# Kernel tuning notes

Hardware: AMD Instinct MI355X
Metric: run time of the kernel (lower is better)

The kernel has to match this reference:

```python
import jax, jax.numpy as jnp
import numpy as np

N = 50000      # nodes
E = 800000     # edges (avg degree 16)
VOCAB = 300    # in_dim = config['vocab_size']
EMBED = 256    # embed_dim
FC = 128       # fc_dim
NCLS = 4       # n_classes_stance
EPS = 1e-12    # F.normalize eps


def setup_inputs() -> dict:
    key = jax.random.key(0)
    ks = jax.random.split(key, 13)
    s_in = 1.0 / np.sqrt(VOCAB)
    s_h = 1.0 / np.sqrt(EMBED)
    s_fc = 1.0 / np.sqrt(FC)
    return {
        "x": jax.random.normal(ks[0], (N, VOCAB), jnp.float32),
        "edge_index": jax.random.randint(ks[1], (2, E), 0, N, dtype=jnp.int32),
        "node_mask": jnp.ones((N, 1), dtype=bool),
        # SAGEConv 1: lin_l (neighbor, with bias) and lin_r (root, no bias)
        "w1_l": jax.random.normal(ks[2], (EMBED, VOCAB), jnp.float32) * s_in,
        "b1_l": jnp.zeros((EMBED,), jnp.float32),
        "w1_r": jax.random.normal(ks[3], (EMBED, VOCAB), jnp.float32) * s_in,
        # SAGEConv 2
        "w2_l": jax.random.normal(ks[4], (EMBED, EMBED), jnp.float32) * s_h,
        "b2_l": jnp.zeros((EMBED,), jnp.float32),
        "w2_r": jax.random.normal(ks[5], (EMBED, EMBED), jnp.float32) * s_h,
        # classifier_stance MLP
        "cw1": jax.random.normal(ks[6], (FC, EMBED), jnp.float32) * s_h,
        "cb1": jnp.zeros((FC,), jnp.float32),
        "cw2": jax.random.normal(ks[7], (NCLS, FC), jnp.float32) * s_fc,
        "cb2": jnp.zeros((NCLS,), jnp.float32),
    }


def _sage_conv(x, src, dst, w_l, b_l, w_r):
    # mean aggregation of source-node features onto destinations
    msg = x[src]                                              # [E, d] gather
    s = jax.ops.segment_sum(msg, dst, num_segments=N)         # [N, d] scatter-add
    cnt = jax.ops.segment_sum(jnp.ones((src.shape[0], 1), x.dtype), dst,
                              num_segments=N)                 # [N, 1]
    agg = s / jnp.maximum(cnt, 1.0)
    h = agg @ w_l.T + b_l + x @ w_r.T                         # lin_l(agg)+lin_r(x)
    # normalize=True -> L2 normalize rows (F.normalize semantics)
    n = jnp.linalg.norm(h, axis=-1, keepdims=True)
    return h / jnp.maximum(n, EPS)


def reference(x, edge_index, node_mask, w1_l, b1_l, w1_r, w2_l, b2_l, w2_r,
              cw1, cb1, cw2, cb2):
    # eval mode: node_drop mask not applied, dropout is identity
    src, dst = edge_index[0], edge_index[1]
    h = jax.nn.relu(_sage_conv(x, src, dst, w1_l, b1_l, w1_r))
    h2 = _sage_conv(h, src, dst, w2_l, b2_l, w2_r)
    out = jax.nn.relu(h2 @ cw1.T + cb1) @ cw2.T + cb2         # classifier_stance
    return (out, node_mask, h2)
```

## Files before the change

kernel.cpp:

```cpp
#include <hip/hip_runtime.h>

constexpr int NN = 50000;
constexpr int MP = 50048;
constexpr int NE = 800000;
constexpr int KV = 300;
constexpr int KP1 = 320;
constexpr int DE = 256;
constexpr int DF = 128;
constexpr int NC = 4;

typedef __attribute__((ext_vector_type(8))) short bf16x8;
typedef __attribute__((ext_vector_type(4))) float f32x4;

__device__ inline float b2f(ushort u) { return __uint_as_float((uint)u << 16); }
__device__ inline ushort f2b(float f) {
    uint u = __float_as_uint(f);
    u += 0x7fffu + ((u >> 16) & 1u);
    return (ushort)(u >> 16);
}
__device__ inline void gload_lds16(const void* g, void* l) {
    __builtin_amdgcn_global_load_lds(
        (const __attribute__((address_space(1))) void*)g,
        (__attribute__((address_space(3))) void*)l, 16, 0, 0);
}

__global__ __launch_bounds__(256) void k_degree(const int* __restrict__ dst,
                                                int* __restrict__ deg) {
    int e = blockIdx.x * 256 + threadIdx.x;
    if (e < NE) atomicAdd(&deg[dst[e]], 1);
}

__global__ __launch_bounds__(256) void k_scan1(const int* __restrict__ deg,
                                               int* __restrict__ partial) {
    __shared__ int sd[256];
    int t = threadIdx.x;
    int n = blockIdx.x * 256 + t;
    sd[t] = (n < NN) ? deg[n] : 0;
    __syncthreads();
    for (int off = 128; off > 0; off >>= 1) {
        if (t < off) sd[t] += sd[t + off];
        __syncthreads();
    }
    if (t == 0) partial[blockIdx.x] = sd[0];
}

__global__ __launch_bounds__(256) void k_scan2(const int* __restrict__ partial,
                                               int* __restrict__ poff, int nb) {
    __shared__ int sd[256];
    int t = threadIdx.x;
    int v = (t < nb) ? partial[t] : 0;
    sd[t] = v;
    __syncthreads();
    for (int off = 1; off < 256; off <<= 1) {
        int x = (t >= off) ? sd[t - off] : 0;
        __syncthreads();
        sd[t] += x;
        __syncthreads();
    }
    poff[t] = sd[t] - v;
}

__global__ __launch_bounds__(256) void k_scan3(const int* __restrict__ deg,
                                               const int* __restrict__ poff,
                                               int* __restrict__ rowptr) {
    __shared__ int sd[256];
    int t = threadIdx.x;
    int n = blockIdx.x * 256 + t;
    int v = (n < NN) ? deg[n] : 0;
    sd[t] = v;
    __syncthreads();
    for (int off = 1; off < 256; off <<= 1) {
        int x = (t >= off) ? sd[t - off] : 0;
        __syncthreads();
        sd[t] += x;
        __syncthreads();
    }
    if (n < NN) rowptr[n] = poff[blockIdx.x] + sd[t] - v;
    if (blockIdx.x == 0 && t == 0) rowptr[NN] = NE;
}

__global__ __launch_bounds__(256) void k_scatter(const int* __restrict__ src,
                                                 const int* __restrict__ dst,
                                                 const int* __restrict__ rowptr,
                                                 int* __restrict__ cnt2,
                                                 int* __restrict__ col) {
    int e = blockIdx.x * 256 + threadIdx.x;
    if (e < NE) {
        int d = dst[e];
        int p = rowptr[d] + atomicAdd(&cnt2[d], 1);
        col[p] = src[e];
    }
}

__global__ __launch_bounds__(256) void k_cvt_x(const float* __restrict__ x,
                                               ushort* __restrict__ xb) {
    int i = blockIdx.x * 256 + threadIdx.x;
    if (i >= MP * (KP1 / 8)) return;
    int row = i / (KP1 / 8);
    int kb = (i % (KP1 / 8)) * 8;
    float f[8] = {0.f, 0.f, 0.f, 0.f, 0.f, 0.f, 0.f, 0.f};
    if (row < NN) {
        const float* s = x + (size_t)row * KV + kb;
        if (kb + 8 <= KV) {
            float4 v0 = *(const float4*)s;
            float4 v1 = *(const float4*)(s + 4);
            f[0] = v0.x; f[1] = v0.y; f[2] = v0.z; f[3] = v0.w;
            f[4] = v1.x; f[5] = v1.y; f[6] = v1.z; f[7] = v1.w;
        } else {
#pragma unroll
            for (int j = 0; j < 8; ++j)
                if (kb + j < KV) f[j] = s[j];
        }
    }
    ushort v[8];
#pragma unroll
    for (int j = 0; j < 8; ++j) v[j] = f2b(f[j]);
    uint4 pk;
    pk.x = (uint)v[0] | ((uint)v[1] << 16);
    pk.y = (uint)v[2] | ((uint)v[3] << 16);
    pk.z = (uint)v[4] | ((uint)v[5] << 16);
    pk.w = (uint)v[6] | ((uint)v[7] << 16);
    *(uint4*)(xb + (size_t)row * KP1 + kb) = pk;
}

__global__ __launch_bounds__(256) void k_cvt_wall(const float* __restrict__ w1l,
                                                  const float* __restrict__ w1r,
                                                  const float* __restrict__ w2l,
                                                  const float* __restrict__ w2r,
                                                  const float* __restrict__ cw1,
                                                  ushort* __restrict__ wcat1,
                                                  ushort* __restrict__ wcat2,
                                                  ushort* __restrict__ cw1b) {
    int i = blockIdx.x * 256 + threadIdx.x;
    const float* src; ushort* dst; int row, kb, Kin;
    if (i < 10240)            { int g = i;          row = g / 40; kb = (g % 40) * 8; src = w1l; dst = wcat1;                       Kin = KV; }
    else if (i < 20480)       { int g = i - 10240;  row = g / 40; kb = (g % 40) * 8; src = w1r; dst = wcat1 + (size_t)256 * KP1;   Kin = KV; }
    else if (i < 28672)       { int g = i - 20480;  row = g / 32; kb = (g % 32) * 8; src = w2l; dst = wcat2;                       Kin = DE; }
    else if (i < 36864)       { int g = i - 28672;  row = g / 32; kb = (g % 32) * 8; src = w2r; dst = wcat2 + (size_t)256 * DE;    Kin = DE; }
    else if (i < 40960)       { int g = i - 36864;  row = g / 32; kb = (g % 32) * 8; src = cw1; dst = cw1b;                        Kin = DE; }
    else return;
    int KPr = (Kin == KV) ? KP1 : DE;
    const float* s = src + (size_t)row * Kin + kb;
    float f[8] = {0.f, 0.f, 0.f, 0.f, 0.f, 0.f, 0.f, 0.f};
    if (kb + 8 <= Kin) {
        float4 v0 = *(const float4*)s;
        float4 v1 = *(const float4*)(s + 4);
        f[0] = v0.x; f[1] = v0.y; f[2] = v0.z; f[3] = v0.w;
        f[4] = v1.x; f[5] = v1.y; f[6] = v1.z; f[7] = v1.w;
    } else {
#pragma unroll
        for (int j = 0; j < 8; ++j)
            if (kb + j < Kin) f[j] = s[j];
    }
    ushort v[8];
#pragma unroll
    for (int j = 0; j < 8; ++j) v[j] = f2b(f[j]);
    uint4 pk;
    pk.x = (uint)v[0] | ((uint)v[1] << 16);
    pk.y = (uint)v[2] | ((uint)v[3] << 16);
    pk.z = (uint)v[4] | ((uint)v[5] << 16);
    pk.w = (uint)v[6] | ((uint)v[7] << 16);
    *(uint4*)(dst + (size_t)row * KPr + kb) = pk;
}

__global__ __launch_bounds__(256) void k_mgemm_layer(const ushort* __restrict__ A,
                                                     const ushort* __restrict__ B,
                                                     unsigned char* __restrict__ ybuf,
                                                     ushort* __restrict__ yrb,
                                                     int KPr) {
    __shared__ __align__(16) ushort As[128 * 64];
    __shared__ __align__(16) ushort Bs[128 * 64];
    const int t = threadIdx.x;
    const int bn = blockIdx.x * 128;
    const int bm = blockIdx.y * 128;
    const int w = t >> 6;
    const int lane = t & 63;
    const int wr = (w >> 1) * 64, wc = (w & 1) * 64;
    const int fr = lane & 15;
    const int fg = lane >> 4;
    const int drow = (lane >> 4) * 4;
    const int dcol = lane & 15;

    f32x4 acc[4][4];
#pragma unroll
    for (int m = 0; m < 4; ++m)
#pragma unroll
        for (int n = 0; n < 4; ++n) acc[m][n] = (f32x4){0.f, 0.f, 0.f, 0.f};

    const int srow = lane >> 3;
    const int sblk = (lane & 7) ^ srow;
    const ushort* Ab = A + (size_t)(bm + w * 32 + srow) * KPr + sblk * 8;
    const ushort* Bb = B + (size_t)(bn + w * 32 + srow) * KPr + sblk * 8;
    ushort* Al = As + w * 2048 + lane * 8;
    ushort* Bl = Bs + w * 2048 + lane * 8;

    for (int k0 = 0; k0 < KPr; k0 += 64) {
#pragma unroll
        for (int j = 0; j < 4; ++j) {
            gload_lds16(Ab + k0 + (size_t)j * 8 * KPr, Al + j * 512);
            gload_lds16(Bb + k0 + (size_t)j * 8 * KPr, Bl + j * 512);
        }
        __syncthreads();
#pragma unroll
        for (int ks = 0; ks < 2; ++ks) {
            bf16x8 af[4], bfr[4];
#pragma unroll
            for (int m = 0; m < 4; ++m) {
                int row = wr + 16 * m + fr;
                int blk = (fg + 4 * ks) ^ (row & 7);
                af[m] = *(const bf16x8*)(As + row * 64 + blk * 8);
            }
#pragma unroll
            for (int n = 0; n < 4; ++n) {
                int row = wc + 16 * n + fr;
                int blk = (fg + 4 * ks) ^ (row & 7);
                bfr[n] = *(const bf16x8*)(Bs + row * 64 + blk * 8);
            }
#pragma unroll
            for (int m = 0; m < 4; ++m)
#pragma unroll
                for (int n = 0; n < 4; ++n)
                    acc[m][n] = __builtin_amdgcn_mfma_f32_16x16x32_bf16(
                        af[m], bfr[n], acc[m][n], 0, 0, 0);
        }
        __syncthreads();
    }
#pragma unroll
    for (int m = 0; m < 4; ++m) {
        int gr0 = bm + wr + 16 * m + drow;
#pragma unroll
        for (int n = 0; n < 4; ++n) {
            int gc = bn + wc + 16 * n + dcol;
#pragma unroll
            for (int r = 0; r < 4; ++r) {
                float v = acc[m][n][r];
                if (gc < 256) {
                    uint p = __builtin_amdgcn_cvt_pk_fp8_f32(v, v, 0, false);
                    ybuf[(size_t)(gr0 + r) * 256 + gc] = (unsigned char)(p & 0xff);
                } else {
                    yrb[(size_t)(gr0 + r) * 256 + (gc - 256)] = f2b(v);
                }
            }
        }
    }
}

__global__ __launch_bounds__(256) void k_mcls(const ushort* __restrict__ A,
                                              const ushort* __restrict__ B,
                                              const float* __restrict__ cb1,
                                              const float* __restrict__ cw2,
                                              const float* __restrict__ cb2,
                                              float* __restrict__ outp) {
    __shared__ __align__(16) ushort smem[128 * 130];
    __shared__ float cw2s[NC * DF];
    ushort* As = smem;
    ushort* Bs = smem + 8192;
    const int t = threadIdx.x;
    const int bm = blockIdx.y * 128;
    const int w = t >> 6;
    const int lane = t & 63;
    const int wr = (w >> 1) * 64, wc = (w & 1) * 64;
    const int fr = lane & 15;
    const int fg = lane >> 4;
    const int drow = (lane >> 4) * 4;
    const int dcol = lane & 15;

    for (int i = t; i < NC * DF; i += 256) cw2s[i] = cw2[i];

    f32x4 acc[4][4];
#pragma unroll
    for (int m = 0; m < 4; ++m)
#pragma unroll
        for (int n = 0; n < 4; ++n) acc[m][n] = (f32x4){0.f, 0.f, 0.f, 0.f};

    const int srow = lane >> 3;
    const int sblk = (lane & 7) ^ srow;
    const ushort* Ab = A + (size_t)(bm + w * 32 + srow) * DE + sblk * 8;
    const ushort* Bb = B + (size_t)(w * 32 + srow) * DE + sblk * 8;
    ushort* Al = As + w * 2048 + lane * 8;
    ushort* Bl = Bs + w * 2048 + lane * 8;

    for (int k0 = 0; k0 < DE; k0 += 64) {
#pragma unroll
        for (int j = 0; j < 4; ++j) {
            gload_lds16(Ab + k0 + (size_t)j * 8 * DE, Al + j * 512);
            gload_lds16(Bb + k0 + (size_t)j * 8 * DE, Bl + j * 512);
        }
        __syncthreads();
#pragma unroll
        for (int ks = 0; ks < 2; ++ks) {
            bf16x8 af[4], bfr[4];
#pragma unroll
            for (int m = 0; m < 4; ++m) {
                int row = wr + 16 * m + fr;
                int blk = (fg + 4 * ks) ^ (row & 7);
                af[m] = *(const bf16x8*)(As + row * 64 + blk * 8);
            }
#pragma unroll
            for (int n = 0; n < 4; ++n) {
                int row = wc + 16 * n + fr;
                int blk = (fg + 4 * ks) ^ (row & 7);
                bfr[n] = *(const bf16x8*)(Bs + row * 64 + blk * 8);
            }
#pragma unroll
            for (int m = 0; m < 4; ++m)
#pragma unroll
                for (int n = 0; n < 4; ++n)
                    acc[m][n] = __builtin_amdgcn_mfma_f32_16x16x32_bf16(
                        af[m], bfr[n], acc[m][n], 0, 0, 0);
        }
        __syncthreads();
    }
#pragma unroll
    for (int m = 0; m < 4; ++m) {
        int lr0 = wr + 16 * m + drow;
#pragma unroll
        for (int n = 0; n < 4; ++n) {
            int f = wc + 16 * n + dcol;
            float bv = cb1[f];
#pragma unroll
            for (int r = 0; r < 4; ++r) {
                float v = fmaxf(acc[m][n][r] + bv, 0.f);
                smem[(lr0 + r) * 130 + f] = f2b(v);
            }
        }
    }
    __syncthreads();
    int node = t >> 1;
    int half = t & 1;
    float p0 = 0.f, p1 = 0.f, p2 = 0.f, p3 = 0.f;
#pragma unroll
    for (int i = 0; i < 32; ++i) {
        uint hv = *(const uint*)&smem[node * 130 + half * 64 + 2 * i];
        float h0 = b2f((ushort)(hv & 0xffff));
        float h1 = b2f((ushort)(hv >> 16));
        int f = half * 64 + 2 * i;
        p0 += h0 * cw2s[0 * DF + f] + h1 * cw2s[0 * DF + f + 1];
        p1 += h0 * cw2s[1 * DF + f] + h1 * cw2s[1 * DF + f + 1];
        p2 += h0 * cw2s[2 * DF + f] + h1 * cw2s[2 * DF + f + 1];
        p3 += h0 * cw2s[3 * DF + f] + h1 * cw2s[3 * DF + f + 1];
    }
    p0 += __shfl_xor(p0, 1, 64);
    p1 += __shfl_xor(p1, 1, 64);
    p2 += __shfl_xor(p2, 1, 64);
    p3 += __shfl_xor(p3, 1, 64);
    int ng = bm + node;
    if (half == 0 && ng < NN) {
        float4 o = make_float4(p0 + cb2[0], p1 + cb2[1], p2 + cb2[2], p3 + cb2[3]);
        *(float4*)(outp + (size_t)ng * NC) = o;
    }
}

__global__ __launch_bounds__(256) void k_aggnorm(const uint* __restrict__ yl,
                                                 const ushort* __restrict__ yrb,
                                                 const float* __restrict__ bias,
                                                 const int* __restrict__ rowptr,
                                                 const int* __restrict__ col,
                                                 float* __restrict__ outf,
                                                 ushort* __restrict__ outb,
                                                 int relu) {
    int wave = threadIdx.x >> 6;
    int lane = threadIdx.x & 63;
    int n = blockIdx.x * 4 + wave;
    if (n >= NN) return;
    int beg = rowptr[n], end = rowptr[n + 1];
    const uint* base = yl + lane;
    float a0 = 0.f, a1 = 0.f, a2 = 0.f, a3 = 0.f;
    float c0 = 0.f, c1 = 0.f, c2 = 0.f, c3 = 0.f;
    int e = beg;
    for (; e + 8 <= end; e += 8) {
        uint v[8];
#pragma unroll
        for (int j = 0; j < 8; ++j) v[j] = base[(size_t)col[e + j] * 64];
#pragma unroll
        for (int j = 0; j < 8; j += 2) {
            a0 += __builtin_amdgcn_cvt_f32_fp8(v[j], 0);
            a1 += __builtin_amdgcn_cvt_f32_fp8(v[j], 1);
            a2 += __builtin_amdgcn_cvt_f32_fp8(v[j], 2);
            a3 += __builtin_amdgcn_cvt_f32_fp8(v[j], 3);
            c0 += __builtin_amdgcn_cvt_f32_fp8(v[j + 1], 0);
            c1 += __builtin_amdgcn_cvt_f32_fp8(v[j + 1], 1);
            c2 += __builtin_amdgcn_cvt_f32_fp8(v[j + 1], 2);
            c3 += __builtin_amdgcn_cvt_f32_fp8(v[j + 1], 3);
        }
    }
    for (; e < end; ++e) {
        uint v = base[(size_t)col[e] * 64];
        a0 += __builtin_amdgcn_cvt_f32_fp8(v, 0);
        a1 += __builtin_amdgcn_cvt_f32_fp8(v, 1);
        a2 += __builtin_amdgcn_cvt_f32_fp8(v, 2);
        a3 += __builtin_amdgcn_cvt_f32_fp8(v, 3);
    }
    a0 += c0; a1 += c1; a2 += c2; a3 += c3;
    int d = end - beg;
    float inv = 1.0f / (float)(d > 1 ? d : 1);
    ushort4 rv = *(const ushort4*)(yrb + (size_t)n * 256 + lane * 4);
    float4 b = *(const float4*)(bias + lane * 4);
    float hx = a0 * inv + b.x + b2f(rv.x);
    float hy = a1 * inv + b.y + b2f(rv.y);
    float hz = a2 * inv + b.z + b2f(rv.z);
    float hw = a3 * inv + b.w + b2f(rv.w);
    float ss = hx * hx + hy * hy + hz * hz + hw * hw;
#pragma unroll
    for (int off = 32; off > 0; off >>= 1) ss += __shfl_xor(ss, off, 64);
    float scale = 1.0f / fmaxf(sqrtf(ss), 1e-12f);
    hx *= scale; hy *= scale; hz *= scale; hw *= scale;
    if (relu) {
        hx = fmaxf(hx, 0.f); hy = fmaxf(hy, 0.f);
        hz = fmaxf(hz, 0.f); hw = fmaxf(hw, 0.f);
    }
    if (outf) {
        float4 o = make_float4(hx, hy, hz, hw);
        *(float4*)(outf + (size_t)n * DE + lane * 4) = o;
    }
    ushort4 ob;
    ob.x = f2b(hx); ob.y = f2b(hy); ob.z = f2b(hz); ob.w = f2b(hw);
    *(ushort4*)(outb + (size_t)n * DE + lane * 4) = ob;
}

__global__ __launch_bounds__(256) void k_mask(const unsigned char* __restrict__ m8,
                                              float* __restrict__ o) {
    int i = blockIdx.x * 256 + threadIdx.x;
    if (i >= NN) return;
    bool bytes = (m8[1] != 0);
    float v;
    if (bytes) v = (m8[i] != 0) ? 1.0f : 0.0f;
    else       v = (((const int*)m8)[i] != 0) ? 1.0f : 0.0f;
    o[i] = v;
}

extern "C" void kernel_launch(void* const* d_in, const int* in_sizes, int n_in,
                              void* d_out, int out_size, void* d_ws, size_t ws_size,
                              hipStream_t stream) {
    const float* x   = (const float*)d_in[0];
    const int*   ei  = (const int*)d_in[1];
    const void*  msk = d_in[2];
    const float* w1l = (const float*)d_in[3];
    const float* b1l = (const float*)d_in[4];
    const float* w1r = (const float*)d_in[5];
    const float* w2l = (const float*)d_in[6];
    const float* b2l = (const float*)d_in[7];
    const float* w2r = (const float*)d_in[8];
    const float* cw1 = (const float*)d_in[9];
    const float* cb1 = (const float*)d_in[10];
    const float* cw2 = (const float*)d_in[11];
    const float* cb2 = (const float*)d_in[12];

    float* out        = (float*)d_out;
    float* out_logits = out;
    float* out_mask   = out + (size_t)NN * NC;
    float* h2f        = out + (size_t)NN * NC + NN;

    char* wp = (char*)d_ws;
    auto alloc = [&](size_t bytes) -> void* {
        void* p = (void*)wp;
        wp += (bytes + 255) & ~(size_t)255;
        return p;
    };
    int* counters = (int*)alloc((size_t)2 * NN * 4);
    int* deg  = counters;
    int* cnt2 = counters + NN;
    int* rowptr  = (int*)alloc((size_t)(NN + 1) * 4);
    int* partial = (int*)alloc(256 * 4);
    int* poff    = (int*)alloc(256 * 4);
    int* col     = (int*)alloc((size_t)NE * 4);
    ushort* xb    = (ushort*)alloc((size_t)MP * KP1 * 2);
    ushort* wcat1 = (ushort*)alloc((size_t)512 * KP1 * 2);
    ushort* wcat2 = (ushort*)alloc((size_t)512 * DE * 2);
    ushort* cw1b  = (ushort*)alloc((size_t)DF * DE * 2);
    unsigned char* ybuf = (unsigned char*)alloc((size_t)MP * 256);
    ushort* yrb   = (ushort*)alloc((size_t)MP * 256 * 2);
    ushort* h1b   = (ushort*)alloc((size_t)MP * DE * 2);
    ushort* h2b   = (ushort*)alloc((size_t)MP * DE * 2);

    const int* srcp = ei;
    const int* dstp = ei + NE;

    hipMemsetAsync(counters, 0, (size_t)2 * NN * 4, stream);
    k_degree<<<(NE + 255) / 256, 256, 0, stream>>>(dstp, deg);
    int nb = (NN + 255) / 256;
    k_scan1<<<nb, 256, 0, stream>>>(deg, partial);
    k_scan2<<<1, 256, 0, stream>>>(partial, poff, nb);
    k_scan3<<<nb, 256, 0, stream>>>(deg, poff, rowptr);
    k_scatter<<<(NE + 255) / 256, 256, 0, stream>>>(srcp, dstp, rowptr, cnt2, col);

    k_cvt_x<<<(MP * (KP1 / 8) + 255) / 256, 256, 0, stream>>>(x, xb);
    k_cvt_wall<<<(40960 + 255) / 256, 256, 0, stream>>>(w1l, w1r, w2l, w2r, cw1,
                                                        wcat1, wcat2, cw1b);

    dim3 g1(512 / 128, MP / 128);
    k_mgemm_layer<<<g1, 256, 0, stream>>>(xb, wcat1, ybuf, yrb, KP1);
    k_aggnorm<<<NN / 4, 256, 0, stream>>>((const uint*)ybuf, yrb, b1l, rowptr, col,
                                          nullptr, h1b, 1);
    k_mgemm_layer<<<g1, 256, 0, stream>>>(h1b, wcat2, ybuf, yrb, DE);
    k_aggnorm<<<NN / 4, 256, 0, stream>>>((const uint*)ybuf, yrb, b2l, rowptr, col,
                                          h2f, h2b, 0);

    dim3 g2(1, MP / 128);
    k_mcls<<<g2, 256, 0, stream>>>(h2b, cw1b, cb1, cw2, cb2, out_logits);
    k_mask<<<(NN + 255) / 256, 256, 0, stream>>>((const unsigned char*)msk, out_mask);
}
```

Before: 401.5 us.

## Fuse independent prep kernels and overlap edge scatter with first GEMM

Merges degree counting with x/weight bf16 conversion into one interleaved launch, and merges the CSR edge scatter, the first-layer GEMM and the mask output into a single kernel whose blocks are interleaved by index. The aim is to cut launch count and let the atomic-bound scatter overlap with compute-bound GEMM tiles instead of running serially. The combined GEMM kernel now reserves shared memory for every block, including the scatter and mask blocks, which may lower occupancy for those blocks.

```diff
diff --git a/kernel.cpp b/kernel.cpp
--- a/kernel.cpp
+++ b/kernel.cpp
@@ -22,12 +22,6 @@
     __builtin_amdgcn_global_load_lds(
         (const __attribute__((address_space(1))) void*)g,
         (__attribute__((address_space(3))) void*)l, 16, 0, 0);
-}
-
-__global__ __launch_bounds__(256) void k_degree(const int* __restrict__ dst,
-                                                int* __restrict__ deg) {
-    int e = blockIdx.x * 256 + threadIdx.x;
-    if (e < NE) atomicAdd(&deg[dst[e]], 1);
 }
 
 __global__ __launch_bounds__(256) void k_scan1(const int* __restrict__ deg,
@@ -79,38 +73,17 @@
     if (blockIdx.x == 0 && t == 0) rowptr[NN] = NE;
 }
 
-__global__ __launch_bounds__(256) void k_scatter(const int* __restrict__ src,
-                                                 const int* __restrict__ dst,
-                                                 const int* __restrict__ rowptr,
-                                                 int* __restrict__ cnt2,
-                                                 int* __restrict__ col) {
-    int e = blockIdx.x * 256 + threadIdx.x;
-    if (e < NE) {
-        int d = dst[e];
-        int p = rowptr[d] + atomicAdd(&cnt2[d], 1);
-        col[p] = src[e];
-    }
-}
-
-__global__ __launch_bounds__(256) void k_cvt_x(const float* __restrict__ x,
-                                               ushort* __restrict__ xb) {
-    int i = blockIdx.x * 256 + threadIdx.x;
-    if (i >= MP * (KP1 / 8)) return;
-    int row = i / (KP1 / 8);
-    int kb = (i % (KP1 / 8)) * 8;
+__device__ inline void cvt8_store(const float* s, int valid, ushort* dptr) {
     float f[8] = {0.f, 0.f, 0.f, 0.f, 0.f, 0.f, 0.f, 0.f};
-    if (row < NN) {
-        const float* s = x + (size_t)row * KV + kb;
-        if (kb + 8 <= KV) {
-            float4 v0 = *(const float4*)s;
-            float4 v1 = *(const float4*)(s + 4);
-            f[0] = v0.x; f[1] = v0.y; f[2] = v0.z; f[3] = v0.w;
-            f[4] = v1.x; f[5] = v1.y; f[6] = v1.z; f[7] = v1.w;
-        } else {
-#pragma unroll
-            for (int j = 0; j < 8; ++j)
-                if (kb + j < KV) f[j] = s[j];
-        }
+    if (valid >= 8) {
+        float4 v0 = *(const float4*)s;
+        float4 v1 = *(const float4*)(s + 4);
+        f[0] = v0.x; f[1] = v0.y; f[2] = v0.z; f[3] = v0.w;
+        f[4] = v1.x; f[5] = v1.y; f[6] = v1.z; f[7] = v1.w;
+    } else {
+#pragma unroll
+        for (int j = 0; j < 8; ++j)
+            if (j < valid) f[j] = s[j];
     }
     ushort v[8];
 #pragma unroll
@@ -120,59 +93,79 @@
     pk.y = (uint)v[2] | ((uint)v[3] << 16);
     pk.z = (uint)v[4] | ((uint)v[5] << 16);
     pk.w = (uint)v[6] | ((uint)v[7] << 16);
-    *(uint4*)(xb + (size_t)row * KP1 + kb) = pk;
-}
-
-__global__ __launch_bounds__(256) void k_cvt_wall(const float* __restrict__ w1l,
-                                                  const float* __restrict__ w1r,
-                                                  const float* __restrict__ w2l,
-                                                  const float* __restrict__ w2r,
-                                                  const float* __restrict__ cw1,
-                                                  ushort* __restrict__ wcat1,
-                                                  ushort* __restrict__ wcat2,
-                                                  ushort* __restrict__ cw1b) {
-    int i = blockIdx.x * 256 + threadIdx.x;
+    *(uint4*)dptr = pk;
+}
+
+__device__ inline void cvt_x_body(int blk, const float* __restrict__ x,
+                                  ushort* __restrict__ xb) {
+    int i = blk * 256 + threadIdx.x;
+    if (i >= MP * (KP1 / 8)) return;
+    int row = i / (KP1 / 8);
+    int kb = (i % (KP1 / 8)) * 8;
+    if (row < NN) {
+        cvt8_store(x + (size_t)row * KV + kb, KV - kb, xb + (size_t)row * KP1 + kb);
+    } else {
+        uint4 z = {0u, 0u, 0u, 0u};
+        *(uint4*)(xb + (size_t)row * KP1 + kb) = z;
+    }
+}
+
+__device__ inline void cvt_wall_body(int blk,
+                                     const float* __restrict__ w1l,
+                                     const float* __restrict__ w1r,
+                                     const float* __restrict__ w2l,
+                                     const float* __restrict__ w2r,
+                                     const float* __restrict__ cw1,
+                                     ushort* __restrict__ wcat1,
+                                     ushort* __restrict__ wcat2,
+                                     ushort* __restrict__ cw1b) {
+    int i = blk * 256 + threadIdx.x;
     const float* src; ushort* dst; int row, kb, Kin;
-    if (i < 10240)            { int g = i;          row = g / 40; kb = (g % 40) * 8; src = w1l; dst = wcat1;                       Kin = KV; }
-    else if (i < 20480)       { int g = i - 10240;  row = g / 40; kb = (g % 40) * 8; src = w1r; dst = wcat1 + (size_t)256 * KP1;   Kin = KV; }
-    else if (i < 28672)       { int g = i - 20480;  row = g / 32; kb = (g % 32) * 8; src = w2l; dst = wcat2;                       Kin = DE; }
-    else if (i < 36864)       { int g = i - 28672;  row = g / 32; kb = (g % 32) * 8; src = w2r; dst = wcat2 + (size_t)256 * DE;    Kin = DE; }
-    else if (i < 40960)       { int g = i - 36864;  row = g / 32; kb = (g % 32) * 8; src = cw1; dst = cw1b;                        Kin = DE; }
+    if (i < 10240)      { int g = i;         row = g / 40; kb = (g % 40) * 8; src = w1l; dst = wcat1;                     Kin = KV; }
+    else if (i < 20480) { int g = i - 10240; row = g / 40; kb = (g % 40) * 8; src = w1r; dst = wcat1 + (size_t)256 * KP1; Kin = KV; }
+    else if (i < 28672) { int g = i - 20480; row = g / 32; kb = (g % 32) * 8; src = w2l; dst = wcat2;                     Kin = DE; }
+    else if (i < 36864) { int g = i - 28672; row = g / 32; kb = (g % 32) * 8; src = w2r; dst = wcat2 + (size_t)256 * DE;  Kin = DE; }
+    else if (i < 40960) { int g = i - 36864; row = g / 32; kb = (g % 32) * 8; src = cw1; dst = cw1b;                      Kin = DE; }
     else return;
     int KPr = (Kin == KV) ? KP1 : DE;
-    const float* s = src + (size_t)row * Kin + kb;
-    float f[8] = {0.f, 0.f, 0.f, 0.f, 0.f, 0.f, 0.f, 0.f};
-    if (kb + 8 <= Kin) {
-        float4 v0 = *(const float4*)s;
-        float4 v1 = *(const float4*)(s + 4);
-        f[0] = v0.x; f[1] = v0.y; f[2] = v0.z; f[3] = v0.w;
-        f[4] = v1.x; f[5] = v1.y; f[6] = v1.z; f[7] = v1.w;
+    cvt8_store(src + (size_t)row * Kin + kb, Kin - kb, dst + (size_t)row * KPr + kb);
+}
+
+__global__ __launch_bounds__(256) void k_prep(const float* __restrict__ x,
+                                              const int* __restrict__ dst,
+                                              const float* __restrict__ w1l,
+                                              const float* __restrict__ w1r,
+                                              const float* __restrict__ w2l,
+                                              const float* __restrict__ w2r,
+                                              const float* __restrict__ cw1,
+                                              ushort* __restrict__ xb,
+                                              ushort* __restrict__ wcat1,
+                                              ushort* __restrict__ wcat2,
+                                              ushort* __restrict__ cw1b,
+                                              int* __restrict__ deg) {
+    int bid = blockIdx.x;
+    int q = bid / 7, r = bid % 7;
+    if (r < 2) {
+        int s = 2 * q + r;
+        if (s < 3125) {
+            int e = s * 256 + threadIdx.x;
+            if (e < NE) atomicAdd(&deg[dst[e]], 1);
+        }
     } else {
-#pragma unroll
-        for (int j = 0; j < 8; ++j)
-            if (kb + j < Kin) f[j] = s[j];
-    }
-    ushort v[8];
-#pragma unroll
-    for (int j = 0; j < 8; ++j) v[j] = f2b(f[j]);
-    uint4 pk;
-    pk.x = (uint)v[0] | ((uint)v[1] << 16);
-    pk.y = (uint)v[2] | ((uint)v[3] << 16);
-    pk.z = (uint)v[4] | ((uint)v[5] << 16);
-    pk.w = (uint)v[6] | ((uint)v[7] << 16);
-    *(uint4*)(dst + (size_t)row * KPr + kb) = pk;
-}
-
-__global__ __launch_bounds__(256) void k_mgemm_layer(const ushort* __restrict__ A,
-                                                     const ushort* __restrict__ B,
-                                                     unsigned char* __restrict__ ybuf,
-                                                     ushort* __restrict__ yrb,
-                                                     int KPr) {
-    __shared__ __align__(16) ushort As[128 * 64];
-    __shared__ __align__(16) ushort Bs[128 * 64];
+        int w = 5 * q + (r - 2);
+        if (w < 7820) cvt_x_body(w, x, xb);
+        else if (w < 7980)
+            cvt_wall_body(w - 7820, w1l, w1r, w2l, w2r, cw1, wcat1, wcat2, cw1b);
+    }
+}
+
+__device__ inline void gemm_layer_body(const ushort* __restrict__ A,
+                                       const ushort* __restrict__ B,
+                                       unsigned char* __restrict__ ybuf,
+                                       ushort* __restrict__ yrb,
+                                       int KPr, int bn, int bm,
+                                       ushort* As, ushort* Bs) {
     const int t = threadIdx.x;
-    const int bn = blockIdx.x * 128;
-    const int bm = blockIdx.y * 128;
     const int w = t >> 6;
     const int lane = t & 63;
     const int wr = (w >> 1) * 64, wc = (w & 1) * 64;
@@ -243,6 +236,125 @@
             }
         }
     }
+}
+
+__global__ __launch_bounds__(256) void k_mgemm_layer(const ushort* __restrict__ A,
+                                                     const ushort* __restrict__ B,
+                                                     unsigned char* __restrict__ ybuf,
+                                                     ushort* __restrict__ yrb,
+                                                     int KPr) {
+    __shared__ __align__(16) ushort As[128 * 64];
+    __shared__ __align__(16) ushort Bs[128 * 64];
+    gemm_layer_body(A, B, ybuf, yrb, KPr, blockIdx.x * 128, blockIdx.y * 128, As, Bs);
+}
+
+__global__ __launch_bounds__(256) void k_g1s(const ushort* __restrict__ A,
+                                             const ushort* __restrict__ B,
+                                             unsigned char* __restrict__ ybuf,
+                                             ushort* __restrict__ yrb,
+                                             const int* __restrict__ src,
+                                             const int* __restrict__ dst,
+                                             const int* __restrict__ rowptr,
+                                             int* __restrict__ cnt2,
+                                             int* __restrict__ col,
+                                             const unsigned char* __restrict__ m8,
+                                             float* __restrict__ omask) {
+    __shared__ __align__(16) ushort As[128 * 64];
+    __shared__ __align__(16) ushort Bs[128 * 64];
+    int bid = blockIdx.x;
+    if (bid < 4692) {
+        int q = bid / 3, r = bid % 3;
+        if (r == 2) {
+            gemm_layer_body(A, B, ybuf, yrb, KP1, (q & 3) * 128, (q >> 2) * 128,
+                            As, Bs);
+        } else {
+            int s = 2 * q + r;
+            if (s < 3125) {
+                int e = s * 256 + threadIdx.x;
+                if (e < NE) {
+                    int d = dst[e];
+                    int p = rowptr[d] + atomicAdd(&cnt2[d], 1);
+                    col[p] = src[e];
+                }
+            }
+        }
+    } else {
+        int i = (bid - 4692) * 256 + threadIdx.x;
+        if (i < NN) {
+            bool bytes = (m8[1] != 0);
+            float v;
+            if (bytes) v = (m8[i] != 0) ? 1.0f : 0.0f;
+            else       v = (((const int*)m8)[i] != 0) ? 1.0f : 0.0f;
+            omask[i] = v;
+        }
+    }
+}
+
+__global__ __launch_bounds__(256) void k_aggnorm(const uint* __restrict__ yl,
+                                                 const ushort* __restrict__ yrb,
+                                                 const float* __restrict__ bias,
+                                                 const int* __restrict__ rowptr,
+                                                 const int* __restrict__ col,
+                                                 float* __restrict__ outf,
+                                                 ushort* __restrict__ outb,
+                                                 int relu) {
+    int wave = threadIdx.x >> 6;
+    int lane = threadIdx.x & 63;
+    int n = blockIdx.x * 4 + wave;
+    if (n >= NN) return;
+    int beg = rowptr[n], end = rowptr[n + 1];
+    const uint* base = yl + lane;
+    float a0 = 0.f, a1 = 0.f, a2 = 0.f, a3 = 0.f;
+    float c0 = 0.f, c1 = 0.f, c2 = 0.f, c3 = 0.f;
+    int e = beg;
+    for (; e + 8 <= end; e += 8) {
+        uint v[8];
+#pragma unroll
+        for (int j = 0; j < 8; ++j) v[j] = base[(size_t)col[e + j] * 64];
+#pragma unroll
+        for (int j = 0; j < 8; j += 2) {
+            a0 += __builtin_amdgcn_cvt_f32_fp8(v[j], 0);
+            a1 += __builtin_amdgcn_cvt_f32_fp8(v[j], 1);
+            a2 += __builtin_amdgcn_cvt_f32_fp8(v[j], 2);
+            a3 += __builtin_amdgcn_cvt_f32_fp8(v[j], 3);
+            c0 += __builtin_amdgcn_cvt_f32_fp8(v[j + 1], 0);
+            c1 += __builtin_amdgcn_cvt_f32_fp8(v[j + 1], 1);
+            c2 += __builtin_amdgcn_cvt_f32_fp8(v[j + 1], 2);
+            c3 += __builtin_amdgcn_cvt_f32_fp8(v[j + 1], 3);
+        }
+    }
+    for (; e < end; ++e) {
+        uint v = base[(size_t)col[e] * 64];
+        a0 += __builtin_amdgcn_cvt_f32_fp8(v, 0);
+        a1 += __builtin_amdgcn_cvt_f32_fp8(v, 1);
+        a2 += __builtin_amdgcn_cvt_f32_fp8(v, 2);
+        a3 += __builtin_amdgcn_cvt_f32_fp8(v, 3);
+    }
+    a0 += c0; a1 += c1; a2 += c2; a3 += c3;
+    int d = end - beg;
+    float inv = 1.0f / (float)(d > 1 ? d : 1);
+    ushort4 rv = *(const ushort4*)(yrb + (size_t)n * 256 + lane * 4);
+    float4 b = *(const float4*)(bias + lane * 4);
+    float hx = a0 * inv + b.x + b2f(rv.x);
+    float hy = a1 * inv + b.y + b2f(rv.y);
+    float hz = a2 * inv + b.z + b2f(rv.z);
+    float hw = a3 * inv + b.w + b2f(rv.w);
+    float ss = hx * hx + hy * hy + hz * hz + hw * hw;
+#pragma unroll
+    for (int off = 32; off > 0; off >>= 1) ss += __shfl_xor(ss, off, 64);
+    float scale = 1.0f / fmaxf(sqrtf(ss), 1e-12f);
+    hx *= scale; hy *= scale; hz *= scale; hw *= scale;
+    if (relu) {
+        hx = fmaxf(hx, 0.f); hy = fmaxf(hy, 0.f);
+        hz = fmaxf(hz, 0.f); hw = fmaxf(hw, 0.f);
+    }
+    if (outf) {
+        float4 o = make_float4(hx, hy, hz, hw);
+        *(float4*)(outf + (size_t)n * DE + lane * 4) = o;
+    }
+    ushort4 ob;
+    ob.x = f2b(hx); ob.y = f2b(hy); ob.z = f2b(hz); ob.w = f2b(hw);
+    *(ushort4*)(outb + (size_t)n * DE + lane * 4) = ob;
 }
 
 __global__ __launch_bounds__(256) void k_mcls(const ushort* __restrict__ A,
@@ -349,84 +461,6 @@
         float4 o = make_float4(p0 + cb2[0], p1 + cb2[1], p2 + cb2[2], p3 + cb2[3]);
         *(float4*)(outp + (size_t)ng * NC) = o;
     }
-}
-
-__global__ __launch_bounds__(256) void k_aggnorm(const uint* __restrict__ yl,
-                                                 const ushort* __restrict__ yrb,
-                                                 const float* __restrict__ bias,
-                                                 const int* __restrict__ rowptr,
-                                                 const int* __restrict__ col,
-                                                 float* __restrict__ outf,
-                                                 ushort* __restrict__ outb,
-                                                 int relu) {
-    int wave = threadIdx.x >> 6;
-    int lane = threadIdx.x & 63;
-    int n = blockIdx.x * 4 + wave;
-    if (n >= NN) return;
-    int beg = rowptr[n], end = rowptr[n + 1];
-    const uint* base = yl + lane;
-    float a0 = 0.f, a1 = 0.f, a2 = 0.f, a3 = 0.f;
-    float c0 = 0.f, c1 = 0.f, c2 = 0.f, c3 = 0.f;
-    int e = beg;
-    for (; e + 8 <= end; e += 8) {
-        uint v[8];
-#pragma unroll
-        for (int j = 0; j < 8; ++j) v[j] = base[(size_t)col[e + j] * 64];
-#pragma unroll
-        for (int j = 0; j < 8; j += 2) {
-            a0 += __builtin_amdgcn_cvt_f32_fp8(v[j], 0);
-            a1 += __builtin_amdgcn_cvt_f32_fp8(v[j], 1);
-            a2 += __builtin_amdgcn_cvt_f32_fp8(v[j], 2);
-            a3 += __builtin_amdgcn_cvt_f32_fp8(v[j], 3);
-            c0 += __builtin_amdgcn_cvt_f32_fp8(v[j + 1], 0);
-            c1 += __builtin_amdgcn_cvt_f32_fp8(v[j + 1], 1);
-            c2 += __builtin_amdgcn_cvt_f32_fp8(v[j + 1], 2);
-            c3 += __builtin_amdgcn_cvt_f32_fp8(v[j + 1], 3);
-        }
-    }
-    for (; e < end; ++e) {
-        uint v = base[(size_t)col[e] * 64];
-        a0 += __builtin_amdgcn_cvt_f32_fp8(v, 0);
-        a1 += __builtin_amdgcn_cvt_f32_fp8(v, 1);
-        a2 += __builtin_amdgcn_cvt_f32_fp8(v, 2);
-        a3 += __builtin_amdgcn_cvt_f32_fp8(v, 3);
-    }
-    a0 += c0; a1 += c1; a2 += c2; a3 += c3;
-    int d = end - beg;
-    float inv = 1.0f / (float)(d > 1 ? d : 1);
-    ushort4 rv = *(const ushort4*)(yrb + (size_t)n * 256 + lane * 4);
-    float4 b = *(const float4*)(bias + lane * 4);
-    float hx = a0 * inv + b.x + b2f(rv.x);
-    float hy = a1 * inv + b.y + b2f(rv.y);
-    float hz = a2 * inv + b.z + b2f(rv.z);
-    float hw = a3 * inv + b.w + b2f(rv.w);
-    float ss = hx * hx + hy * hy + hz * hz + hw * hw;
-#pragma unroll
-    for (int off = 32; off > 0; off >>= 1) ss += __shfl_xor(ss, off, 64);
-    float scale = 1.0f / fmaxf(sqrtf(ss), 1e-12f);
-    hx *= scale; hy *= scale; hz *= scale; hw *= scale;
-    if (relu) {
-        hx = fmaxf(hx, 0.f); hy = fmaxf(hy, 0.f);
-        hz = fmaxf(hz, 0.f); hw = fmaxf(hw, 0.f);
-    }
-    if (outf) {
-        float4 o = make_float4(hx, hy, hz, hw);
-        *(float4*)(outf + (size_t)n * DE + lane * 4) = o;
-    }
-    ushort4 ob;
-    ob.x = f2b(hx); ob.y = f2b(hy); ob.z = f2b(hz); ob.w = f2b(hw);
-    *(ushort4*)(outb + (size_t)n * DE + lane * 4) = ob;
-}
-
-__global__ __launch_bounds__(256) void k_mask(const unsigned char* __restrict__ m8,
-                                              float* __restrict__ o) {
-    int i = blockIdx.x * 256 + threadIdx.x;
-    if (i >= NN) return;
-    bool bytes = (m8[1] != 0);
-    float v;
-    if (bytes) v = (m8[i] != 0) ? 1.0f : 0.0f;
-    else       v = (((const int*)m8)[i] != 0) ? 1.0f : 0.0f;
-    o[i] = v;
 }
 
 extern "C" void kernel_launch(void* const* d_in, const int* in_sizes, int n_in,
@@ -477,26 +511,22 @@
     const int* dstp = ei + NE;
 
     hipMemsetAsync(counters, 0, (size_t)2 * NN * 4, stream);
-    k_degree<<<(NE + 255) / 256, 256, 0, stream>>>(dstp, deg);
+    k_prep<<<11270, 256, 0, stream>>>(x, dstp, w1l, w1r, w2l, w2r, cw1,
+                                      xb, wcat1, wcat2, cw1b, deg);
     int nb = (NN + 255) / 256;
     k_scan1<<<nb, 256, 0, stream>>>(deg, partial);
     k_scan2<<<1, 256, 0, stream>>>(partial, poff, nb);
     k_scan3<<<nb, 256, 0, stream>>>(deg, poff, rowptr);
-    k_scatter<<<(NE + 255) / 256, 256, 0, stream>>>(srcp, dstp, rowptr, cnt2, col);
-
-    k_cvt_x<<<(MP * (KP1 / 8) + 255) / 256, 256, 0, stream>>>(x, xb);
-    k_cvt_wall<<<(40960 + 255) / 256, 256, 0, stream>>>(w1l, w1r, w2l, w2r, cw1,
-                                                        wcat1, wcat2, cw1b);
-
-    dim3 g1(512 / 128, MP / 128);
-    k_mgemm_layer<<<g1, 256, 0, stream>>>(xb, wcat1, ybuf, yrb, KP1);
+
+    k_g1s<<<4888, 256, 0, stream>>>(xb, wcat1, ybuf, yrb, srcp, dstp, rowptr,
+                                    cnt2, col, (const unsigned char*)msk, out_mask);
     k_aggnorm<<<NN / 4, 256, 0, stream>>>((const uint*)ybuf, yrb, b1l, rowptr, col,
                                           nullptr, h1b, 1);
+    dim3 g1(512 / 128, MP / 128);
     k_mgemm_layer<<<g1, 256, 0, stream>>>(h1b, wcat2, ybuf, yrb, DE);
     k_aggnorm<<<NN / 4, 256, 0, stream>>>((const uint*)ybuf, yrb, b2l, rowptr, col,
                                           h2f, h2b, 0);
 
     dim3 g2(1, MP / 128);
     k_mcls<<<g2, 256, 0, stream>>>(h2b, cw1b, cb1, cw2, cb2, out_logits);
-    k_mask<<<(NN + 255) / 256, 256, 0, stream>>>((const unsigned char*)msk, out_mask);
-}
+}
```

After: 424.0 us. 1.06x slower.
